# Kernel tuning notes

Measured on AMD Instinct MI355X. Metric: run time of the kernel, lower is better.

## Reference

```python
import jax, jax.numpy as jnp
import numpy as np

QDEPTH = 8
WIDTH = 64
HEIGHT = 64
WIRES = 12  # ceil(log2(64*64))
BATCH = 1024


def setup_inputs() -> dict:
    key = jax.random.key(0)
    k1, k2 = jax.random.split(key)
    x = jax.random.normal(k1, (BATCH, 1, WIDTH, HEIGHT), dtype=jnp.float32)
    # torch.nn.Parameter(torch.randn(weight_shape) * 0.4)
    weights = jax.random.normal(k2, (QDEPTH, WIRES, 3), dtype=jnp.float32) * 0.4
    return {"x": x, "weights": weights, "reps": 1}


def _rot_matrices(angles):
    # angles: (L, W, 3) -> (L, W, 2, 2) complex64; Rot(phi, theta, omega) = RZ(omega) RY(theta) RZ(phi)
    phi, theta, omega = angles[..., 0], angles[..., 1], angles[..., 2]
    c = jnp.cos(theta * 0.5).astype(jnp.complex64)
    s = jnp.sin(theta * 0.5).astype(jnp.complex64)
    ep = jnp.exp(-0.5j * (phi + omega).astype(jnp.complex64))  # e^{-i(phi+omega)/2}
    em = jnp.exp(-0.5j * (phi - omega).astype(jnp.complex64))  # e^{-i(phi-omega)/2}
    row0 = jnp.stack([ep * c, -jnp.conj(em) * s], axis=-1)
    row1 = jnp.stack([em * s, jnp.conj(ep) * c], axis=-1)
    return jnp.stack([row0, row1], axis=-2)


def _apply_1q(state, U, wire):
    # state: (B, 2, 2, ..., 2); apply 2x2 U on axis wire+1
    ax = wire + 1
    s = jnp.moveaxis(state, ax, -1)
    s = s @ U.T  # out[..., i] = sum_j U[i, j] s[..., j]
    return jnp.moveaxis(s, -1, ax)


def _apply_cnot(state, control, target):
    c, t = control + 1, target + 1
    s0, s1 = jnp.split(state, 2, axis=c)   # control = 0 / 1 halves
    s1 = jnp.flip(s1, axis=t)              # X on target where control = 1
    return jnp.concatenate([s0, s1], axis=c)


def _sel_layer(state, mats_l, r):
    # one StronglyEntanglingLayers layer: Rot on every wire, then CNOT ring of range r
    for w in range(WIRES):
        state = _apply_1q(state, mats_l[w], w)
    for w in range(WIRES):
        state = _apply_cnot(state, w, (w + r) % WIRES)
    return state


def _circuit(state, weights, reps):
    mats = _rot_matrices(jnp.tanh(weights))  # qw_map.tanh applied to raw weights
    for _ in range(reps):
        for l in range(QDEPTH):
            r = (l % (WIRES - 1)) + 1  # PennyLane default ranges
            layer = jax.checkpoint(lambda s, m, _r=r: _sel_layer(s, m, _r))
            state = layer(state, mats[l])
    return state


def reference(x, weights, reps):
    b = x.shape[0]
    v = x.reshape(b, -1)  # (b, 4096)
    norm = jnp.linalg.norm(v, axis=-1, keepdims=True)
    v = (v / norm).astype(jnp.complex64)
    state = v.reshape((b,) + (2,) * WIRES)
    state = _circuit(state, weights, reps)
    out = state.reshape(b, -1) * norm
    return out.reshape(b, 1, WIDTH, HEIGHT)
```

## Files before the change

kernel.cpp:

```cpp
#include <hip/hip_runtime.h>

#define WIRES   12
#define NSTATE  4096
#define QDEPTH  8
#define BLOCK   64
#define PER_T   64

using f2 = __attribute__((ext_vector_type(2))) float;

__device__ __forceinline__ int pad(int i) { return i + (i >> 6); }

constexpr int colF(int l, int j) {
    int rr = (l % (WIRES - 1)) + 1;
    int v = 1 << j;
    for (int k = WIRES - 1; k >= 0; --k) {
        int bc = 11 - k;
        int bt = 11 - ((k + rr) % WIRES);
        v ^= ((v >> bc) & 1) << bt;
    }
    return v;
}
struct ColsT { int v[QDEPTH][WIRES]; };
constexpr ColsT mkCols() {
    ColsT c{};
    for (int l = 0; l < QDEPTH; ++l)
        for (int j = 0; j < WIRES; ++j) c.v[l][j] = colF(l, j);
    return c;
}
static __device__ const ColsT COLS = mkCols();

__global__ void mats_kernel(const float* __restrict__ wts, f2* __restrict__ mg)
{
    int t = blockIdx.x * blockDim.x + threadIdx.x;
    if (t >= QDEPTH * WIRES) return;
    float phi   = tanhf(wts[t * 3 + 0]);
    float theta = tanhf(wts[t * 3 + 1]);
    float omega = tanhf(wts[t * 3 + 2]);
    float c  = cosf(theta * 0.5f);
    float s  = sinf(theta * 0.5f);
    float a  = 0.5f * (phi + omega);
    float bm = 0.5f * (phi - omega);
    float ca = cosf(a),  sa = sinf(a);
    float cb = cosf(bm), sb = sinf(bm);
    f2* m = mg + t * 8;
    m[0] = f2{ c * ca,  c * ca};
    m[1] = f2{ c * sa, -c * sa};
    m[2] = f2{-s * cb, -s * cb};
    m[3] = f2{ s * sb, -s * sb};
    m[4] = f2{ s * cb,  s * cb};
    m[5] = f2{ s * sb, -s * sb};
    m[6] = f2{ c * ca,  c * ca};
    m[7] = f2{-c * sa,  c * sa};
}

template<int P>
__device__ __forceinline__ void gate(f2 r[PER_T], const f2* __restrict__ m)
{
    const f2 u00r = m[0], u00w = m[1], u01r = m[2], u01w = m[3];
    const f2 u10r = m[4], u10w = m[5], u11r = m[6], u11w = m[7];
    #pragma unroll
    for (int pr = 0; pr < PER_T / 2; pr += 2) {
        const int k0 = ((pr >> P) << (P + 1)) | (pr & ((1 << P) - 1));
        const int k1 = k0 | (1 << P);
        const int q  = pr + 1;
        const int j0 = ((q >> P) << (P + 1)) | (q & ((1 << P) - 1));
        const int j1 = j0 | (1 << P);
        f2 a0, b0, a1, b1;
        asm("v_pk_mul_f32 %0, %4, %8\n\t"
            "v_pk_mul_f32 %1, %4, %12\n\t"
            "v_pk_mul_f32 %2, %6, %8\n\t"
            "v_pk_mul_f32 %3, %6, %12\n\t"
            "v_pk_fma_f32 %0, %4, %9, %0 op_sel:[1,0,0] op_sel_hi:[0,1,1]\n\t"
            "v_pk_fma_f32 %1, %4, %13, %1 op_sel:[1,0,0] op_sel_hi:[0,1,1]\n\t"
            "v_pk_fma_f32 %2, %6, %9, %2 op_sel:[1,0,0] op_sel_hi:[0,1,1]\n\t"
            "v_pk_fma_f32 %3, %6, %13, %3 op_sel:[1,0,0] op_sel_hi:[0,1,1]\n\t"
            "v_pk_fma_f32 %0, %5, %10, %0\n\t"
            "v_pk_fma_f32 %1, %5, %14, %1\n\t"
            "v_pk_fma_f32 %2, %7, %10, %2\n\t"
            "v_pk_fma_f32 %3, %7, %14, %3\n\t"
            "v_pk_fma_f32 %0, %5, %11, %0 op_sel:[1,0,0] op_sel_hi:[0,1,1]\n\t"
            "v_pk_fma_f32 %1, %5, %15, %1 op_sel:[1,0,0] op_sel_hi:[0,1,1]\n\t"
            "v_pk_fma_f32 %2, %7, %11, %2 op_sel:[1,0,0] op_sel_hi:[0,1,1]\n\t"
            "v_pk_fma_f32 %3, %7, %15, %3 op_sel:[1,0,0] op_sel_hi:[0,1,1]"
            : "=&v"(a0), "=&v"(b0), "=&v"(a1), "=&v"(b1)
            : "v"(r[k0]), "v"(r[k1]), "v"(r[j0]), "v"(r[j1]),
              "v"(u00r), "v"(u00w), "v"(u01r), "v"(u01w),
              "v"(u10r), "v"(u10w), "v"(u11r), "v"(u11w));
        r[k0] = a0; r[k1] = b0; r[j0] = a1; r[j1] = b1;
    }
}

__global__ __launch_bounds__(BLOCK, 1) void qsim_kernel(
    const float* __restrict__ x,
    const f2*    __restrict__ mats_g,
    const int*   __restrict__ reps_ptr,
    float*       __restrict__ out,
    int write_mode)
{
    __shared__ f2 st[65 * 64];

    const int lane = threadIdx.x;
    const int b    = blockIdx.x;

    const float4* xb4 = (const float4*)(x + (size_t)b * NSTATE);
    #pragma unroll
    for (int c = 0; c < 16; ++c) {
        int g = c * BLOCK + lane;
        float4 v = xb4[g];
        st[pad(2 * g)]     = f2{v.x, v.y};
        st[pad(2 * g + 1)] = f2{v.z, v.w};
    }
    f2 r[PER_T];
    #pragma unroll
    for (int m = 0; m < 32; ++m) {
        f2 pr2 = st[pad((lane << 5) | m)];
        r[2*m]   = f2{pr2.x, 0.f};
        r[2*m+1] = f2{pr2.y, 0.f};
    }

    const int reps = reps_ptr[0];
    for (int rep = 0; rep < reps; ++rep) {
        #pragma unroll 1
        for (int l = 0; l < QDEPTH; ++l) {
            const f2* M = mats_g + l * WIRES * 8;

            gate<5>(r, M + 6*8);  gate<4>(r, M + 7*8);
            gate<3>(r, M + 8*8);  gate<2>(r, M + 9*8);
            gate<1>(r, M + 10*8); gate<0>(r, M + 11*8);

            #pragma unroll
            for (int k = 0; k < PER_T; ++k) st[65 * lane + k] = r[k];
            #pragma unroll
            for (int k = 0; k < PER_T; ++k) r[k] = st[65 * k + lane];

            gate<5>(r, M + 0*8); gate<4>(r, M + 1*8);
            gate<3>(r, M + 2*8); gate<2>(r, M + 3*8);
            gate<1>(r, M + 4*8); gate<0>(r, M + 5*8);

            #pragma unroll
            for (int k = 0; k < PER_T; ++k) st[65 * k + lane] = r[k];

            const int c0 = COLS.v[l][0], c1 = COLS.v[l][1], c2 = COLS.v[l][2];
            const int c3 = COLS.v[l][3], c4 = COLS.v[l][4], c5 = COLS.v[l][5];
            int Ft = 0;
            #pragma unroll
            for (int j = 0; j < 6; ++j)
                Ft ^= ((lane >> j) & 1) ? COLS.v[l][6 + j] : 0;
            #pragma unroll
            for (int k = 0; k < PER_T; ++k) {
                int ck = ((k & 1)  ? c0 : 0) ^ ((k & 2)  ? c1 : 0) ^
                         ((k & 4)  ? c2 : 0) ^ ((k & 8)  ? c3 : 0) ^
                         ((k & 16) ? c4 : 0) ^ ((k & 32) ? c5 : 0);
                r[k] = st[pad(Ft ^ ck)];
            }
        }
    }

    if (write_mode == 0) {
        #pragma unroll
        for (int m = 0; m < 32; ++m)
            st[pad((lane << 5) | m)] = f2{r[2*m].x, r[2*m+1].x};
        float4* ob4 = (float4*)(out + (size_t)b * NSTATE);
        #pragma unroll
        for (int c = 0; c < 16; ++c) {
            int g = c * BLOCK + lane;
            f2 a  = st[pad(2 * g)];
            f2 b2 = st[pad(2 * g + 1)];
            ob4[g] = make_float4(a.x, a.y, b2.x, b2.y);
        }
    } else {
        float2* ob = (float2*)out + (size_t)b * NSTATE;
        #pragma unroll
        for (int k = 0; k < PER_T; ++k)
            ob[(lane << 6) | k] = make_float2(r[k].x, r[k].y);
    }
}

extern "C" void kernel_launch(void* const* d_in, const int* in_sizes, int n_in,
                              void* d_out, int out_size, void* d_ws, size_t ws_size,
                              hipStream_t stream) {
    const float* x    = (const float*)d_in[0];
    const float* wts  = (const float*)d_in[1];
    const int*   reps = (const int*)d_in[2];
    float*       out  = (float*)d_out;
    f2*          mg   = (f2*)d_ws;
    (void)in_sizes; (void)n_in; (void)ws_size;

    const int write_mode = (out_size >= 2 * 1024 * NSTATE) ? 1 : 0;

    mats_kernel<<<1, 128, 0, stream>>>(wts, mg);
    qsim_kernel<<<1024, BLOCK, 0, stream>>>(x, mg, reps, out, write_mode);
}
```

Measured before the change: 154.0 us.

## Split each state vector across 256 threads with three-stage shared-memory transposes

Each batch element's 4096-amplitude state is now spread over 256 threads holding 16 amplitudes each, where before it was 64 threads holding 64 each. Each layer's twelve rotations become three groups of four register-local gates, separated by padded shared-memory transposes and block barriers. The CNOT permutation is applied through a gather indexed by an 8-bit thread index. The goal is less register pressure and higher occupancy (up to 4 blocks per CU) so latency is hidden better. The cost is an extra transpose and several __syncthreads per layer.

```diff
diff --git a/kernel.cpp b/kernel.cpp
--- a/kernel.cpp
+++ b/kernel.cpp
@@ -3,12 +3,12 @@
 #define WIRES   12
 #define NSTATE  4096
 #define QDEPTH  8
-#define BLOCK   64
-#define PER_T   64
+#define BLOCK   256
+#define PER_T   16
 
 using f2 = __attribute__((ext_vector_type(2))) float;
 
-__device__ __forceinline__ int pad(int i) { return i + (i >> 6); }
+__device__ __forceinline__ int slotf(int a) { return a + (a >> 4); }
 
 constexpr int colF(int l, int j) {
     int rr = (l % (WIRES - 1)) + 1;
@@ -90,32 +90,31 @@
     }
 }
 
-__global__ __launch_bounds__(BLOCK, 1) void qsim_kernel(
+__global__ __launch_bounds__(BLOCK, 4) void qsim_kernel(
     const float* __restrict__ x,
     const f2*    __restrict__ mats_g,
     const int*   __restrict__ reps_ptr,
     float*       __restrict__ out,
     int write_mode)
 {
-    __shared__ f2 st[65 * 64];
+    __shared__ f2 st[4352];
 
-    const int lane = threadIdx.x;
-    const int b    = blockIdx.x;
+    const int g   = threadIdx.x;
+    const int b   = blockIdx.x;
+    const int ghi = g >> 4, glo = g & 15;
+    const int w1b = 17 * g;
+    const int rb1 = 272 * ghi + glo;
+    const int rb2 = 17 * ghi + glo;
 
-    const float4* xb4 = (const float4*)(x + (size_t)b * NSTATE);
-    #pragma unroll
-    for (int c = 0; c < 16; ++c) {
-        int g = c * BLOCK + lane;
-        float4 v = xb4[g];
-        st[pad(2 * g)]     = f2{v.x, v.y};
-        st[pad(2 * g + 1)] = f2{v.z, v.w};
-    }
+    const float4* xb4 = (const float4*)(x + (size_t)b * NSTATE) + g * 4;
     f2 r[PER_T];
     #pragma unroll
-    for (int m = 0; m < 32; ++m) {
-        f2 pr2 = st[pad((lane << 5) | m)];
-        r[2*m]   = f2{pr2.x, 0.f};
-        r[2*m+1] = f2{pr2.y, 0.f};
+    for (int c = 0; c < 4; ++c) {
+        float4 v = xb4[c];
+        r[4*c+0] = f2{v.x, 0.f};
+        r[4*c+1] = f2{v.y, 0.f};
+        r[4*c+2] = f2{v.z, 0.f};
+        r[4*c+3] = f2{v.w, 0.f};
     }
 
     const int reps = reps_ptr[0];
@@ -124,55 +123,57 @@
         for (int l = 0; l < QDEPTH; ++l) {
             const f2* M = mats_g + l * WIRES * 8;
 
-            gate<5>(r, M + 6*8);  gate<4>(r, M + 7*8);
             gate<3>(r, M + 8*8);  gate<2>(r, M + 9*8);
             gate<1>(r, M + 10*8); gate<0>(r, M + 11*8);
 
             #pragma unroll
-            for (int k = 0; k < PER_T; ++k) st[65 * lane + k] = r[k];
+            for (int k = 0; k < PER_T; ++k) st[w1b + k] = r[k];
+            __syncthreads();
             #pragma unroll
-            for (int k = 0; k < PER_T; ++k) r[k] = st[65 * k + lane];
+            for (int k = 0; k < PER_T; ++k) r[k] = st[rb1 + 17 * k];
 
-            gate<5>(r, M + 0*8); gate<4>(r, M + 1*8);
-            gate<3>(r, M + 2*8); gate<2>(r, M + 3*8);
-            gate<1>(r, M + 4*8); gate<0>(r, M + 5*8);
+            gate<3>(r, M + 4*8); gate<2>(r, M + 5*8);
+            gate<1>(r, M + 6*8); gate<0>(r, M + 7*8);
 
             #pragma unroll
-            for (int k = 0; k < PER_T; ++k) st[65 * k + lane] = r[k];
+            for (int k = 0; k < PER_T; ++k) st[rb1 + 17 * k] = r[k];
+            __syncthreads();
+            #pragma unroll
+            for (int k = 0; k < PER_T; ++k) r[k] = st[rb2 + 272 * k];
 
-            const int c0 = COLS.v[l][0], c1 = COLS.v[l][1], c2 = COLS.v[l][2];
-            const int c3 = COLS.v[l][3], c4 = COLS.v[l][4], c5 = COLS.v[l][5];
-            int Ft = 0;
+            gate<3>(r, M + 0*8); gate<2>(r, M + 1*8);
+            gate<1>(r, M + 2*8); gate<0>(r, M + 3*8);
+
             #pragma unroll
-            for (int j = 0; j < 6; ++j)
-                Ft ^= ((lane >> j) & 1) ? COLS.v[l][6 + j] : 0;
+            for (int k = 0; k < PER_T; ++k) st[rb2 + 272 * k] = r[k];
+            __syncthreads();
+
+            int Fg = 0;
+            #pragma unroll
+            for (int j = 0; j < 8; ++j)
+                Fg ^= ((g >> j) & 1) ? COLS.v[l][4 + j] : 0;
+            const int c0 = COLS.v[l][0], c1 = COLS.v[l][1];
+            const int c2 = COLS.v[l][2], c3 = COLS.v[l][3];
             #pragma unroll
             for (int k = 0; k < PER_T; ++k) {
-                int ck = ((k & 1)  ? c0 : 0) ^ ((k & 2)  ? c1 : 0) ^
-                         ((k & 4)  ? c2 : 0) ^ ((k & 8)  ? c3 : 0) ^
-                         ((k & 16) ? c4 : 0) ^ ((k & 32) ? c5 : 0);
-                r[k] = st[pad(Ft ^ ck)];
+                int ck = ((k & 1) ? c0 : 0) ^ ((k & 2) ? c1 : 0) ^
+                         ((k & 4) ? c2 : 0) ^ ((k & 8) ? c3 : 0);
+                r[k] = st[slotf(Fg ^ ck)];
             }
+            __syncthreads();
         }
     }
 
     if (write_mode == 0) {
+        float4* ob4 = (float4*)(out + (size_t)b * NSTATE) + g * 4;
         #pragma unroll
-        for (int m = 0; m < 32; ++m)
-            st[pad((lane << 5) | m)] = f2{r[2*m].x, r[2*m+1].x};
-        float4* ob4 = (float4*)(out + (size_t)b * NSTATE);
+        for (int c = 0; c < 4; ++c)
+            ob4[c] = make_float4(r[4*c].x, r[4*c+1].x, r[4*c+2].x, r[4*c+3].x);
+    } else {
+        float4* ob4 = (float4*)((float2*)out + (size_t)b * NSTATE) + g * 8;
         #pragma unroll
-        for (int c = 0; c < 16; ++c) {
-            int g = c * BLOCK + lane;
-            f2 a  = st[pad(2 * g)];
-            f2 b2 = st[pad(2 * g + 1)];
-            ob4[g] = make_float4(a.x, a.y, b2.x, b2.y);
-        }
-    } else {
-        float2* ob = (float2*)out + (size_t)b * NSTATE;
-        #pragma unroll
-        for (int k = 0; k < PER_T; ++k)
-            ob[(lane << 6) | k] = make_float2(r[k].x, r[k].y);
+        for (int k = 0; k < PER_T; k += 2)
+            ob4[k >> 1] = make_float4(r[k].x, r[k].y, r[k+1].x, r[k+1].y);
     }
 }
 
```

New measurement: 145.6 us. 1.06x faster.
